# Optimization experiments

Hardware: AMD Instinct MI355X
Metric: run time of the kernel (lower is better)

The kernel has to match this reference:

```python
import jax, jax.numpy as jnp
import numpy as np

B, N, D, E, H = 128, 64, 128, 32, 256

def setup_inputs() -> dict:
    key = jax.random.key(0)
    ks = jax.random.split(key, 6)
    nodes = jax.random.normal(ks[0], (B, N, D), dtype=jnp.float32)
    edges = jax.random.normal(ks[1], (B, N * N, E), dtype=jnp.float32)
    W1 = jax.random.normal(ks[2], (2 * D + E, H), dtype=jnp.float32) * (1.0 / np.sqrt(2 * D + E))
    b1 = jnp.zeros((H,), dtype=jnp.float32)
    W2 = jax.random.normal(ks[3], (H, H), dtype=jnp.float32) * (1.0 / np.sqrt(H))
    b2 = jnp.zeros((H,), dtype=jnp.float32)
    W3 = jax.random.normal(ks[4], (H, 1), dtype=jnp.float32) * (1.0 / np.sqrt(H))
    b3 = jnp.zeros((1,), dtype=jnp.float32)
    return {"nodes": nodes, "edges": edges, "W1": W1, "b1": b1, "W2": W2, "b2": b2, "W3": W3, "b3": b3}

def reference(nodes, edges, W1, b1, W2, b2, W3, b3):
    b, n, d = nodes.shape
    # state_i[p] = nodes[p // n] (each node repeated n times consecutively)
    state_i = jnp.broadcast_to(nodes[:, :, None, :], (b, n, n, d)).reshape(b, n * n, d)
    # state_j[p] = nodes[p % n] (whole node list tiled n times)
    state_j = jnp.broadcast_to(nodes[:, None, :, :], (b, n, n, d)).reshape(b, n * n, d)
    concat = jnp.concatenate([state_i, edges, state_j], axis=-1)  # [b, n*n, 2d+e]
    a1 = jax.nn.relu(jnp.einsum('bpf,fh->bph', concat, W1) + b1)
    a2 = jax.nn.relu(jnp.einsum('bph,hk->bpk', a1, W2) + b2)
    return jnp.einsum('bph,ho->bpo', a2, W3) + b3  # [b, n*n, 1]
```

## Files before the change

kernel.cpp:

```cpp
#include <hip/hip_runtime.h>
#include <hip/hip_bf16.h>

typedef __bf16 bf16_t;
typedef __bf16 bf16x8 __attribute__((ext_vector_type(8)));
typedef float  f32x4  __attribute__((ext_vector_type(4)));

static __device__ __forceinline__ f32x4 mfma16(bf16x8 a, bf16x8 b, f32x4 c) {
    return __builtin_amdgcn_mfma_f32_16x16x32_bf16(a, b, c, 0, 0, 0);
}

__global__ void prep_pack(const float* __restrict__ W1, const float* __restrict__ W2,
                          bf16_t* __restrict__ W1ef, bf16_t* __restrict__ W2f) {
    int t = blockIdx.x * blockDim.x + threadIdx.x;
    int l = t & 63, g = l >> 4, c = l & 15;
    if (t < 1024) {
        int ht = t >> 6;
        int hcol = 32 * (ht >> 1) + 8 * (c >> 2) + 4 * (ht & 1) + (c & 3);
        #pragma unroll
        for (int j = 0; j < 8; ++j)
            W1ef[t * 8 + j] = (bf16_t)W1[(128 + 8 * g + j) * 256 + hcol];
    } else if (t < 1024 + 8192) {
        int t2 = t - 1024;
        int ks = t2 >> 10;
        int ct = (t2 >> 6) & 15;
        #pragma unroll
        for (int j = 0; j < 8; ++j) {
            int krow = 32 * ks + 8 * g + 4 * (j >> 2) + (j & 3);
            W2f[t2 * 8 + j] = (bf16_t)W2[krow * 256 + ct * 16 + c];
        }
    }
}

__global__ __launch_bounds__(256) void prep_pij(const float* __restrict__ nodes,
                                                const float* __restrict__ W1,
                                                const float* __restrict__ b1,
                                                float* __restrict__ Pi,
                                                bf16_t* __restrict__ Pjb) {
    int b = blockIdx.x >> 3;
    int q = blockIdx.x & 7;
    int h = threadIdx.x;
    const float* nb = nodes + (b * 64 + q * 8) * 128;
    float ai[8], aj[8];
    float bias = b1[h];
    #pragma unroll
    for (int ii = 0; ii < 8; ++ii) { ai[ii] = bias; aj[ii] = 0.f; }
    for (int d = 0; d < 128; ++d) {
        float wi = W1[d * 256 + h];
        float wj = W1[(160 + d) * 256 + h];
        #pragma unroll
        for (int ii = 0; ii < 8; ++ii) {
            float s = nb[ii * 128 + d];
            ai[ii] = fmaf(s, wi, ai[ii]);
            aj[ii] = fmaf(s, wj, aj[ii]);
        }
    }
    #pragma unroll
    for (int ii = 0; ii < 8; ++ii) {
        Pi[(b * 64 + q * 8 + ii) * 256 + h] = ai[ii];
        Pjb[(b * 64 + q * 8 + ii) * 256 + h] = (bf16_t)aj[ii];
    }
}

__global__ __launch_bounds__(512, 2) void mlp_main(
    const float* __restrict__ edges,
    const float* __restrict__ Pi, const bf16_t* __restrict__ Pjb,
    const bf16_t* __restrict__ W1ef, const bf16_t* __restrict__ W2f,
    const float* __restrict__ b2, const float* __restrict__ W3,
    const float* __restrict__ b3, float* __restrict__ out) {

    __shared__ bf16_t a1f[2][16384];
    __shared__ bf16_t elds[2][2048];
    __shared__ float part[2][8][64];

    const int p = blockIdx.x;
    const int xb = (p & 7) * 64 + (p >> 3);
    const int tid = threadIdx.x;
    const int w = tid >> 6, l = tid & 63, g = l >> 4, c = l & 15;
    const int b = xb >> 2;
    const f32x4 z4 = {0.f, 0.f, 0.f, 0.f};

    bf16x8 wf[2];
    #pragma unroll
    for (int z = 0; z < 2; ++z)
        wf[z] = *(const bf16x8*)&W1ef[((2 * w + z) * 64 + l) * 8];

    bf16x8 pjb[4];
    #pragma unroll
    for (int pt = 0; pt < 4; ++pt)
        pjb[pt] = *(const bf16x8*)&Pjb[((long)(b * 64 + 16 * pt + c)) * 256
                                       + 32 * w + 8 * g];

    const float bias3 = b3[0];

    const int spt = tid >> 6, sg = (tid >> 4) & 3, sc = tid & 15;
    const long erowbase = (long)xb * 1024 + 16 * spt + sc;

    f32x4 es0, es1;
    if (tid < 256) {
        const float* ep = edges + erowbase * 32 + 8 * sg;
        es0 = *(const f32x4*)ep; es1 = *(const f32x4*)(ep + 4);
    }
    const float* PiB = Pi + ((long)xb * 16) * 256 + 32 * w + 8 * g;
    f32x4 pva0 = *(const f32x4*)PiB;
    f32x4 pva1 = *(const f32x4*)(PiB + 4);

    if (tid < 256) {
        bf16x8 ev;
        #pragma unroll
        for (int j = 0; j < 4; ++j) { ev[j] = (bf16_t)es0[j]; ev[4 + j] = (bf16_t)es1[j]; }
        *(bf16x8*)&elds[0][tid * 8] = ev;
    }
    __syncthreads();

    f32x4 pvb0, pvb1;

    for (int t = 0; t < 16; ++t) {
        const int cur = t & 1;

        if (t < 15) {
            if (tid < 256) {
                const float* ep = edges + (erowbase + 64 * (t + 1)) * 32 + 8 * sg;
                es0 = *(const f32x4*)ep; es1 = *(const f32x4*)(ep + 4);
            }
            const float* pp = PiB + (t + 1) * 256;
            pvb0 = *(const f32x4*)pp; pvb1 = *(const f32x4*)(pp + 4);
        }

        {
            bf16x8 ebf[4];
            #pragma unroll
            for (int pt = 0; pt < 4; ++pt)
                ebf[pt] = *(const bf16x8*)&elds[cur][(pt * 64 + l) * 8];
            #pragma unroll
            for (int pt = 0; pt < 4; ++pt) {
                bf16x8 o;
                #pragma unroll
                for (int z = 0; z < 2; ++z) {
                    f32x4 a = mfma16(wf[z], ebf[pt], z4);
                    f32x4 pv = z ? pva1 : pva0;
                    #pragma unroll
                    for (int r = 0; r < 4; ++r) {
                        float v = a[r] + pv[r] + (float)pjb[pt][4 * z + r];
                        v = v > 0.f ? v : 0.f;
                        o[4 * z + r] = (bf16_t)v;
                    }
                }
                *(bf16x8*)&a1f[cur][((pt * 8 + w) * 64 + l) * 8] = o;
            }
        }

        if (t < 15 && tid < 256) {
            bf16x8 ev;
            #pragma unroll
            for (int j = 0; j < 4; ++j) { ev[j] = (bf16_t)es0[j]; ev[4 + j] = (bf16_t)es1[j]; }
            *(bf16x8*)&elds[cur ^ 1][tid * 8] = ev;
        }
        __syncthreads();

        if (t > 0 && tid < 64) {
            float s = bias3;
            #pragma unroll
            for (int ww = 0; ww < 8; ++ww) s += part[cur ^ 1][ww][tid];
            out[(long)xb * 1024 + (t - 1) * 64 + tid] = s;
        }

        {
            f32x4 acc2[4][2];
            #pragma unroll
            for (int pt = 0; pt < 4; ++pt) { acc2[pt][0] = z4; acc2[pt][1] = z4; }

            __builtin_amdgcn_s_setprio(1);
            #pragma unroll
            for (int ks = 0; ks < 8; ++ks) {
                bf16x8 af[4];
                #pragma unroll
                for (int pt = 0; pt < 4; ++pt)
                    af[pt] = *(const bf16x8*)&a1f[cur][((pt * 8 + ks) * 64 + l) * 8];
                #pragma unroll
                for (int cc = 0; cc < 2; ++cc) {
                    bf16x8 w2 = *(const bf16x8*)&W2f[((ks * 16 + 2 * w + cc) * 64 + l) * 8];
                    #pragma unroll
                    for (int pt = 0; pt < 4; ++pt)
                        acc2[pt][cc] = mfma16(w2, af[pt], acc2[pt][cc]);
                }
            }
            __builtin_amdgcn_s_setprio(0);

            f32x4 b2q[2], w3q[2];
            #pragma unroll
            for (int cc = 0; cc < 2; ++cc) {
                b2q[cc] = *(const f32x4*)&b2[32 * w + 16 * cc + 4 * g];
                w3q[cc] = *(const f32x4*)&W3[32 * w + 16 * cc + 4 * g];
            }
            #pragma unroll
            for (int pt = 0; pt < 4; ++pt) {
                float s = 0.f;
                #pragma unroll
                for (int cc = 0; cc < 2; ++cc)
                    #pragma unroll
                    for (int r = 0; r < 4; ++r) {
                        float v = acc2[pt][cc][r] + b2q[cc][r];
                        v = v > 0.f ? v : 0.f;
                        s = fmaf(v, w3q[cc][r], s);
                    }
                s += __shfl_xor(s, 16);
                s += __shfl_xor(s, 32);
                if (g == 0) part[cur][w][pt * 16 + c] = s;
            }
        }
        pva0 = pvb0; pva1 = pvb1;
    }

    __syncthreads();
    if (tid < 64) {
        float s = bias3;
        #pragma unroll
        for (int ww = 0; ww < 8; ++ww) s += part[1][ww][tid];
        out[(long)xb * 1024 + 15 * 64 + tid] = s;
    }
}

extern "C" void kernel_launch(void* const* d_in, const int* in_sizes, int n_in,
                              void* d_out, int out_size, void* d_ws, size_t ws_size,
                              hipStream_t stream) {
    const float* nodes = (const float*)d_in[0];
    const float* edges = (const float*)d_in[1];
    const float* W1    = (const float*)d_in[2];
    const float* b1    = (const float*)d_in[3];
    const float* W2    = (const float*)d_in[4];
    const float* b2    = (const float*)d_in[5];
    const float* W3    = (const float*)d_in[6];
    const float* b3    = (const float*)d_in[7];
    float* out = (float*)d_out;

    char* ws = (char*)d_ws;
    float*  Pi   = (float*)ws;
    bf16_t* Pjb  = (bf16_t*)(ws + (size_t)8 * 1024 * 1024);
    bf16_t* W2f  = (bf16_t*)(ws + (size_t)12 * 1024 * 1024);
    bf16_t* W1ef = (bf16_t*)(ws + (size_t)12 * 1024 * 1024 + 131072);

    prep_pack<<<dim3(36), dim3(256), 0, stream>>>(W1, W2, W1ef, W2f);
    prep_pij<<<dim3(1024), dim3(256), 0, stream>>>(nodes, W1, b1, Pi, Pjb);
    mlp_main<<<dim3(512), dim3(512), 0, stream>>>(edges, Pi, Pjb, W1ef, W2f, b2, W3, b3, out);
}
```

Before: 104.4 us.

## Software-pipeline layer1 and layer2 phases with one barrier per iteration

```diff
diff --git a/kernel.cpp b/kernel.cpp
--- a/kernel.cpp
+++ b/kernel.cpp
@@ -78,6 +78,8 @@
     const int w = tid >> 6, l = tid & 63, g = l >> 4, c = l & 15;
     const int b = xb >> 2;
     const f32x4 z4 = {0.f, 0.f, 0.f, 0.f};
+    const float bias3 = b3[0];
+    const long outbase = (long)xb * 1024;
 
     bf16x8 wf[2];
     #pragma unroll
@@ -90,133 +92,136 @@
         pjb[pt] = *(const bf16x8*)&Pjb[((long)(b * 64 + 16 * pt + c)) * 256
                                        + 32 * w + 8 * g];
 
-    const float bias3 = b3[0];
+    const float* PiB = Pi + ((long)xb * 16) * 256 + 32 * w + 8 * g;
 
     const int spt = tid >> 6, sg = (tid >> 4) & 3, sc = tid & 15;
     const long erowbase = (long)xb * 1024 + 16 * spt + sc;
+
+    auto PHASE_A = [&](int tt, int buf) {
+        const float* pp = PiB + tt * 256;
+        f32x4 pva0 = *(const f32x4*)pp;
+        f32x4 pva1 = *(const f32x4*)(pp + 4);
+        bf16x8 ebf[4];
+        #pragma unroll
+        for (int pt = 0; pt < 4; ++pt)
+            ebf[pt] = *(const bf16x8*)&elds[buf][(pt * 64 + l) * 8];
+        #pragma unroll
+        for (int pt = 0; pt < 4; ++pt) {
+            bf16x8 o;
+            #pragma unroll
+            for (int z = 0; z < 2; ++z) {
+                f32x4 a = mfma16(wf[z], ebf[pt], z4);
+                f32x4 pv = z ? pva1 : pva0;
+                #pragma unroll
+                for (int r = 0; r < 4; ++r) {
+                    float v = a[r] + pv[r] + (float)pjb[pt][4 * z + r];
+                    v = v > 0.f ? v : 0.f;
+                    o[4 * z + r] = (bf16_t)v;
+                }
+            }
+            *(bf16x8*)&a1f[buf][((pt * 8 + w) * 64 + l) * 8] = o;
+        }
+    };
+
+    auto PHASE_B = [&](int buf) {
+        f32x4 acc2[4][2];
+        #pragma unroll
+        for (int pt = 0; pt < 4; ++pt) { acc2[pt][0] = z4; acc2[pt][1] = z4; }
+        #pragma unroll
+        for (int ks = 0; ks < 8; ++ks) {
+            bf16x8 af[4];
+            #pragma unroll
+            for (int pt = 0; pt < 4; ++pt)
+                af[pt] = *(const bf16x8*)&a1f[buf][((pt * 8 + ks) * 64 + l) * 8];
+            #pragma unroll
+            for (int cc = 0; cc < 2; ++cc) {
+                bf16x8 w2 = *(const bf16x8*)&W2f[((ks * 16 + 2 * w + cc) * 64 + l) * 8];
+                #pragma unroll
+                for (int pt = 0; pt < 4; ++pt)
+                    acc2[pt][cc] = mfma16(w2, af[pt], acc2[pt][cc]);
+            }
+        }
+        f32x4 b2q[2], w3q[2];
+        #pragma unroll
+        for (int cc = 0; cc < 2; ++cc) {
+            b2q[cc] = *(const f32x4*)&b2[32 * w + 16 * cc + 4 * g];
+            w3q[cc] = *(const f32x4*)&W3[32 * w + 16 * cc + 4 * g];
+        }
+        #pragma unroll
+        for (int pt = 0; pt < 4; ++pt) {
+            float s = 0.f;
+            #pragma unroll
+            for (int cc = 0; cc < 2; ++cc)
+                #pragma unroll
+                for (int r = 0; r < 4; ++r) {
+                    float v = acc2[pt][cc][r] + b2q[cc][r];
+                    v = v > 0.f ? v : 0.f;
+                    s = fmaf(v, w3q[cc][r], s);
+                }
+            s += __shfl_xor(s, 16);
+            s += __shfl_xor(s, 32);
+            if (g == 0) part[buf][w][pt * 16 + c] = s;
+        }
+    };
 
     f32x4 es0, es1;
     if (tid < 256) {
         const float* ep = edges + erowbase * 32 + 8 * sg;
-        es0 = *(const f32x4*)ep; es1 = *(const f32x4*)(ep + 4);
-    }
-    const float* PiB = Pi + ((long)xb * 16) * 256 + 32 * w + 8 * g;
-    f32x4 pva0 = *(const f32x4*)PiB;
-    f32x4 pva1 = *(const f32x4*)(PiB + 4);
-
+        f32x4 a0 = *(const f32x4*)ep, a1 = *(const f32x4*)(ep + 4);
+        bf16x8 ev;
+        #pragma unroll
+        for (int j = 0; j < 4; ++j) { ev[j] = (bf16_t)a0[j]; ev[4 + j] = (bf16_t)a1[j]; }
+        *(bf16x8*)&elds[0][tid * 8] = ev;
+        const float* ep1 = edges + (erowbase + 64) * 32 + 8 * sg;
+        es0 = *(const f32x4*)ep1; es1 = *(const f32x4*)(ep1 + 4);
+    }
+    __syncthreads();
+
+    PHASE_A(0, 0);
     if (tid < 256) {
         bf16x8 ev;
         #pragma unroll
         for (int j = 0; j < 4; ++j) { ev[j] = (bf16_t)es0[j]; ev[4 + j] = (bf16_t)es1[j]; }
-        *(bf16x8*)&elds[0][tid * 8] = ev;
-    }
-    __syncthreads();
-
-    f32x4 pvb0, pvb1;
-
-    for (int t = 0; t < 16; ++t) {
+        *(bf16x8*)&elds[1][tid * 8] = ev;
+    }
+
+    for (int t = 0; t < 15; ++t) {
+        __syncthreads();
         const int cur = t & 1;
-
-        if (t < 15) {
-            if (tid < 256) {
-                const float* ep = edges + (erowbase + 64 * (t + 1)) * 32 + 8 * sg;
-                es0 = *(const f32x4*)ep; es1 = *(const f32x4*)(ep + 4);
-            }
-            const float* pp = PiB + (t + 1) * 256;
-            pvb0 = *(const f32x4*)pp; pvb1 = *(const f32x4*)(pp + 4);
-        }
-
-        {
-            bf16x8 ebf[4];
-            #pragma unroll
-            for (int pt = 0; pt < 4; ++pt)
-                ebf[pt] = *(const bf16x8*)&elds[cur][(pt * 64 + l) * 8];
-            #pragma unroll
-            for (int pt = 0; pt < 4; ++pt) {
-                bf16x8 o;
-                #pragma unroll
-                for (int z = 0; z < 2; ++z) {
-                    f32x4 a = mfma16(wf[z], ebf[pt], z4);
-                    f32x4 pv = z ? pva1 : pva0;
-                    #pragma unroll
-                    for (int r = 0; r < 4; ++r) {
-                        float v = a[r] + pv[r] + (float)pjb[pt][4 * z + r];
-                        v = v > 0.f ? v : 0.f;
-                        o[4 * z + r] = (bf16_t)v;
-                    }
-                }
-                *(bf16x8*)&a1f[cur][((pt * 8 + w) * 64 + l) * 8] = o;
-            }
-        }
-
-        if (t < 15 && tid < 256) {
-            bf16x8 ev;
-            #pragma unroll
-            for (int j = 0; j < 4; ++j) { ev[j] = (bf16_t)es0[j]; ev[4 + j] = (bf16_t)es1[j]; }
-            *(bf16x8*)&elds[cur ^ 1][tid * 8] = ev;
-        }
-        __syncthreads();
-
+        if (t < 14 && tid < 256) {
+            const float* ep = edges + (erowbase + 64 * (t + 2)) * 32 + 8 * sg;
+            es0 = *(const f32x4*)ep; es1 = *(const f32x4*)(ep + 4);
+        }
         if (t > 0 && tid < 64) {
             float s = bias3;
             #pragma unroll
             for (int ww = 0; ww < 8; ++ww) s += part[cur ^ 1][ww][tid];
-            out[(long)xb * 1024 + (t - 1) * 64 + tid] = s;
-        }
-
-        {
-            f32x4 acc2[4][2];
-            #pragma unroll
-            for (int pt = 0; pt < 4; ++pt) { acc2[pt][0] = z4; acc2[pt][1] = z4; }
-
-            __builtin_amdgcn_s_setprio(1);
-            #pragma unroll
-            for (int ks = 0; ks < 8; ++ks) {
-                bf16x8 af[4];
-                #pragma unroll
-                for (int pt = 0; pt < 4; ++pt)
-                    af[pt] = *(const bf16x8*)&a1f[cur][((pt * 8 + ks) * 64 + l) * 8];
-                #pragma unroll
-                for (int cc = 0; cc < 2; ++cc) {
-                    bf16x8 w2 = *(const bf16x8*)&W2f[((ks * 16 + 2 * w + cc) * 64 + l) * 8];
-                    #pragma unroll
-                    for (int pt = 0; pt < 4; ++pt)
-                        acc2[pt][cc] = mfma16(w2, af[pt], acc2[pt][cc]);
-                }
-            }
-            __builtin_amdgcn_s_setprio(0);
-
-            f32x4 b2q[2], w3q[2];
-            #pragma unroll
-            for (int cc = 0; cc < 2; ++cc) {
-                b2q[cc] = *(const f32x4*)&b2[32 * w + 16 * cc + 4 * g];
-                w3q[cc] = *(const f32x4*)&W3[32 * w + 16 * cc + 4 * g];
-            }
-            #pragma unroll
-            for (int pt = 0; pt < 4; ++pt) {
-                float s = 0.f;
-                #pragma unroll
-                for (int cc = 0; cc < 2; ++cc)
-                    #pragma unroll
-                    for (int r = 0; r < 4; ++r) {
-                        float v = acc2[pt][cc][r] + b2q[cc][r];
-                        v = v > 0.f ? v : 0.f;
-                        s = fmaf(v, w3q[cc][r], s);
-                    }
-                s += __shfl_xor(s, 16);
-                s += __shfl_xor(s, 32);
-                if (g == 0) part[cur][w][pt * 16 + c] = s;
-            }
-        }
-        pva0 = pvb0; pva1 = pvb1;
+            out[outbase + (t - 1) * 64 + tid] = s;
+        }
+        PHASE_B(cur);
+        PHASE_A(t + 1, cur ^ 1);
+        if (t < 14 && tid < 256) {
+            bf16x8 ev;
+            #pragma unroll
+            for (int j = 0; j < 4; ++j) { ev[j] = (bf16_t)es0[j]; ev[4 + j] = (bf16_t)es1[j]; }
+            *(bf16x8*)&elds[cur][tid * 8] = ev;
+        }
     }
 
     __syncthreads();
     if (tid < 64) {
         float s = bias3;
         #pragma unroll
+        for (int ww = 0; ww < 8; ++ww) s += part[0][ww][tid];
+        out[outbase + 14 * 64 + tid] = s;
+    }
+    PHASE_B(1);
+    __syncthreads();
+    if (tid < 64) {
+        float s = bias3;
+        #pragma unroll
         for (int ww = 0; ww < 8; ++ww) s += part[1][ww][tid];
-        out[(long)xb * 1024 + 15 * 64 + tid] = s;
+        out[outbase + 15 * 64 + tid] = s;
     }
 }
 
```

Result: slower. 110.4 us (+5.7%).
